# Kernel tuning notes

Hardware: AMD Instinct MI355X
Metric: run time of the kernel (lower is better)

Reference implementation:

```python
import jax, jax.numpy as jnp
import numpy as np

N_NODES = 50000
N_EDGES = 800000
IN_DIM, HID_DIM, N_CLASS = 128, 128, 2
DROPOUT_P = 0.5
NEG_SLOPE = 0.01  # F.leaky_relu default


def gcn_conv(x, src, dst, W, b, n_nodes):
    """PyG GCNConv: add self-loops, sym-normalize, aggregate, then bias."""
    loops = jnp.arange(n_nodes, dtype=src.dtype)
    s = jnp.concatenate([src, loops])
    d = jnp.concatenate([dst, loops])
    # degree on A + I (edge weights = 1), counted at destination
    deg = jax.ops.segment_sum(jnp.ones_like(d, dtype=x.dtype), d, num_segments=n_nodes)
    dis = jnp.where(deg > 0, jax.lax.rsqrt(deg), 0.0)  # deg^{-1/2}
    norm = dis[s] * dis[d]                               # [E+N]
    h = x @ W                                            # [N, out]
    msg = h[s] * norm[:, None]                           # gather + scale
    out = jax.ops.segment_sum(msg, d, num_segments=n_nodes)  # scatter-add
    return out + b


def dropout(x, p, key):
    keep = 1.0 - p
    mask = jax.random.bernoulli(key, keep, x.shape)
    return jnp.where(mask, x / keep, 0.0)


def setup_inputs() -> dict:
    key = jax.random.key(0)
    ks = jax.random.split(key, 8)
    x = jax.random.normal(ks[0], (N_NODES, IN_DIM), dtype=jnp.float32)
    edge_index = jax.random.randint(ks[1], (2, N_EDGES), 0, N_NODES, dtype=jnp.int64)
    def glorot(k, fin, fout):
        lim = np.sqrt(6.0 / (fin + fout)).astype(np.float32)
        return jax.random.uniform(k, (fin, fout), jnp.float32, -lim, lim)
    W1 = glorot(ks[2], IN_DIM, HID_DIM)
    W2 = glorot(ks[3], HID_DIM, HID_DIM)
    W3 = glorot(ks[4], HID_DIM, N_CLASS)
    b1 = jnp.zeros((HID_DIM,), jnp.float32)
    b2 = jnp.zeros((HID_DIM,), jnp.float32)
    b3 = jnp.zeros((N_CLASS,), jnp.float32)
    return {"x": x, "edge_index": edge_index, "W1": W1, "b1": b1,
            "W2": W2, "b2": b2, "W3": W3, "b3": b3}


def reference(x, edge_index, W1, b1, W2, b2, W3, b3):
    src, dst = edge_index[0], edge_index[1]
    n = x.shape[0]
    dkey = jax.random.key(42)
    k1, k2 = jax.random.split(dkey)
    h = gcn_conv(x, src, dst, W1, b1, n)
    h = jax.nn.leaky_relu(h, NEG_SLOPE)
    h = dropout(h, DROPOUT_P, k1)
    h = gcn_conv(h, src, dst, W2, b2, n)
    h = jax.nn.leaky_relu(h, NEG_SLOPE)
    h = dropout(h, DROPOUT_P, k2)
    h = gcn_conv(h, src, dst, W3, b3, n)
    return jax.nn.log_softmax(h, axis=1)
```

## Files before the change

### kernel.cpp

```cpp
#include <hip/hip_runtime.h>
#include <stdint.h>

#define N_NODES 50000
#define N_EDGES 800000
#define DIM     128
#define NB   196
#define CAP  8192
#define CHUNK 2048
#define NBLK 391
#define GCAP 4096
#define G3CAP 8192

typedef __attribute__((ext_vector_type(8))) unsigned short ushort8_t;
typedef __attribute__((ext_vector_type(8))) short bfrag;
typedef __attribute__((ext_vector_type(4))) float f32x4;

__host__ __device__ inline void threefry2x32(uint32_t k0, uint32_t k1,
                                             uint32_t x0, uint32_t x1,
                                             uint32_t& o0, uint32_t& o1) {
    uint32_t ks0 = k0, ks1 = k1, ks2 = k0 ^ k1 ^ 0x1BD11BDAu;
    uint32_t v0 = x0 + ks0, v1 = x1 + ks1;
#define TF_R(r) { v0 += v1; v1 = (v1 << (r)) | (v1 >> (32 - (r))); v1 ^= v0; }
    TF_R(13) TF_R(15) TF_R(26) TF_R(6)
    v0 += ks1; v1 += ks2 + 1u;
    TF_R(17) TF_R(29) TF_R(16) TF_R(24)
    v0 += ks2; v1 += ks0 + 2u;
    TF_R(13) TF_R(15) TF_R(26) TF_R(6)
    v0 += ks0; v1 += ks1 + 3u;
    TF_R(17) TF_R(29) TF_R(16) TF_R(24)
    v0 += ks1; v1 += ks2 + 4u;
    TF_R(13) TF_R(15) TF_R(26) TF_R(6)
    v0 += ks2; v1 += ks0 + 5u;
#undef TF_R
    o0 = v0; o1 = v1;
}

__device__ inline float drop_scale(uint32_t kk0, uint32_t kk1, uint32_t i) {
    uint32_t b0, b1;
    threefry2x32(kk0, kk1, 0u, i, b0, b1);
    uint32_t bits = b0 ^ b1;
    return (bits >> 31) ? 0.0f : 2.0f;
}

__device__ inline float bf2f(ushort u) {
    return __uint_as_float(((uint32_t)u) << 16);
}

__device__ inline ushort f2bf_rne(float f) {
    uint32_t bits = __float_as_uint(f);
    uint32_t lsb = (bits >> 16) & 1u;
    bits += 0x7fffu + lsb;
    return (ushort)(bits >> 16);
}

template<int F32A>
__device__ inline void gemm_body(const ushort* __restrict__ Xb,
                                 const float* __restrict__ Xf,
                                 const ushort* __restrict__ Wt,
                                 const float* __restrict__ dis,
                                 ushort* __restrict__ Hb, int gb, int tid) {
    int w = tid >> 6, lane = tid & 63;
    int m0 = gb * 128 + w * 32;
    int lrow = lane & 15, quad = lane >> 4;
    f32x4 acc[2][8] = {};
    for (int kt = 0; kt < DIM; kt += 32) {
        bfrag a[2], b[8];
        #pragma unroll
        for (int t = 0; t < 2; ++t) {
            int m = m0 + t * 16 + lrow;
            if (m >= N_NODES) m = 0;
            if (F32A) {
                const float* p = Xf + (size_t)m * DIM + kt + quad * 8;
                f32x4 v0 = *(const f32x4*)p;
                f32x4 v1 = *(const f32x4*)(p + 4);
                #pragma unroll
                for (int j = 0; j < 4; ++j) {
                    a[t][j]     = (short)f2bf_rne(v0[j]);
                    a[t][j + 4] = (short)f2bf_rne(v1[j]);
                }
            } else {
                a[t] = *(const bfrag*)(Xb + (size_t)m * DIM + kt + quad * 8);
            }
        }
        #pragma unroll
        for (int c = 0; c < 8; ++c) {
            int n = c * 16 + lrow;
            b[c] = *(const bfrag*)(Wt + (size_t)n * DIM + kt + quad * 8);
        }
        #pragma unroll
        for (int t = 0; t < 2; ++t)
            #pragma unroll
            for (int c = 0; c < 8; ++c)
                acc[t][c] = __builtin_amdgcn_mfma_f32_16x16x32_bf16(a[t], b[c], acc[t][c], 0, 0, 0);
    }
    #pragma unroll
    for (int t = 0; t < 2; ++t) {
        #pragma unroll
        for (int r = 0; r < 4; ++r) {
            int rowi = m0 + t * 16 + quad * 4 + r;
            if (rowi < N_NODES) {
                float dv = dis[rowi];
                #pragma unroll
                for (int c = 0; c < 8; ++c) {
                    int feat = c * 16 + lrow;
                    int fp = feat >> 5, off = feat & 31;
                    Hb[((size_t)fp * N_NODES + rowi) * 32 + off] = f2bf_rne(acc[t][c][r] * dv);
                }
            }
        }
    }
}

__global__ __launch_bounds__(256) void k_prep(const float* __restrict__ W1,
                                              const float* __restrict__ W2,
                                              ushort* __restrict__ W1t,
                                              ushort* __restrict__ W2t,
                                              const int* __restrict__ src,
                                              const int* __restrict__ dst,
                                              uint32_t* __restrict__ gcur,
                                              uint32_t* __restrict__ packed) {
    __shared__ uint32_t h[NB];
    int b = blockIdx.x;
    int t = threadIdx.x;
    if (b < NBLK) {
        uint32_t dc[CHUNK / 256], sc[CHUNK / 256];
        if (t < NB) h[t] = 0u;
        __syncthreads();
        int base = b * CHUNK;
        #pragma unroll
        for (int i = 0; i < CHUNK / 256; ++i) {
            int e = base + i * 256 + t;
            if (e < N_EDGES) {
                dc[i] = (uint32_t)dst[e];
                sc[i] = (uint32_t)src[e];
                atomicAdd(&h[dc[i] >> 8], 1u);
            } else {
                dc[i] = 0xffffffffu;
            }
        }
        __syncthreads();
        if (t < NB) {
            uint32_t c = h[t];
            h[t] = c ? atomicAdd(&gcur[t], c) : 0u;
        }
        __syncthreads();
        #pragma unroll
        for (int i = 0; i < CHUNK / 256; ++i) {
            if (dc[i] != 0xffffffffu) {
                uint32_t d = dc[i];
                uint32_t s = sc[i];
                uint32_t bk = d >> 8;
                uint32_t pos = atomicAdd(&h[bk], 1u);
                if (pos < CAP)
                    packed[(size_t)bk * CAP + pos] = ((d & 255u) << 16) | s;
            }
        }
    } else {
        int j = (b - NBLK) * 256 + t;
        const float* W = (j < DIM * DIM) ? W1 : W2;
        ushort* Wt = (j < DIM * DIM) ? W1t : W2t;
        int i = j & (DIM * DIM - 1);
        int k = i >> 7, n = i & 127;
        Wt[n * DIM + k] = f2bf_rne(W[k * DIM + n]);
    }
}

__global__ __launch_bounds__(256) void k_fill(const uint32_t* __restrict__ gcur,
                                              const uint32_t* __restrict__ packed,
                                              uint32_t* __restrict__ row,
                                              float* __restrict__ dis,
                                              ushort* __restrict__ col16) {
    __shared__ uint32_t sdeg[256];
    __shared__ uint32_t scan[256];
    __shared__ uint32_t cur[256];
    int b = blockIdx.x;
    int t = threadIdx.x;
    uint32_t n = gcur[b];
    scan[t] = (t < b) ? gcur[t] : 0u;
    __syncthreads();
    for (int off = 1; off < 256; off <<= 1) {
        uint32_t x = (t >= off) ? scan[t - off] : 0u;
        __syncthreads();
        scan[t] += x;
        __syncthreads();
    }
    uint32_t cbase = scan[255];
    __syncthreads();
    uint32_t pbase = (uint32_t)b * CAP;
    sdeg[t] = 0u;
    __syncthreads();
    for (uint32_t i = t; i < n; i += 256) {
        uint32_t u = packed[pbase + i];
        atomicAdd(&sdeg[u >> 16], 1u);
    }
    __syncthreads();
    uint32_t myd = sdeg[t];
    scan[t] = myd;
    __syncthreads();
    for (int off = 1; off < 256; off <<= 1) {
        uint32_t x = (t >= off) ? scan[t - off] : 0u;
        __syncthreads();
        scan[t] += x;
        __syncthreads();
    }
    uint32_t excl = scan[t] - myd;
    cur[t] = excl;
    int v = b * 256 + t;
    if (v <= N_NODES) row[v] = cbase + excl;
    if (v < N_NODES)  dis[v] = 1.0f / sqrtf((float)(myd + 1u));
    __syncthreads();
    for (uint32_t i = t; i < n; i += 256) {
        uint32_t u = packed[pbase + i];
        uint32_t pos = cbase + atomicAdd(&cur[u >> 16], 1u);
        col16[pos] = (ushort)(u & 0xffffu);
    }
}

template<int CLS>
__global__ __launch_bounds__(256) void k_gather_t(const uint32_t* __restrict__ row,
                                                  const ushort* __restrict__ col16,
                                                  const float* __restrict__ dis,
                                                  const ushort* __restrict__ Hb,
                                                  const float* __restrict__ bias,
                                                  ushort* __restrict__ OUTb,
                                                  const float* __restrict__ W3,
                                                  float* __restrict__ h3s,
                                                  uint32_t kk0, uint32_t kk1) {
    __shared__ ushort scol[GCAP];
    __shared__ uint32_t srow[65];
    int fp = blockIdx.x & 3;
    int c = blockIdx.x >> 2;
    int tid = threadIdx.x;
    int nbase = c * 64;
    int nend = nbase + 64; if (nend > N_NODES) nend = N_NODES;
    int nloc = nend - nbase;
    for (int i = tid; i <= nloc; i += 256) srow[i] = row[nbase + i];
    __syncthreads();
    uint32_t eLo = srow[0];
    uint32_t count = srow[nloc] - eLo;
    bool staged = count <= GCAP;
    if (staged) {
        for (uint32_t i = tid; i < count; i += 256) scol[i] = col16[eLo + i];
    }
    __syncthreads();

    int nl = tid >> 2;
    int q  = tid & 3;
    int v = nbase + nl;
    if (v >= N_NODES) return;
    const ushort* Hf = Hb + (size_t)fp * N_NODES * 32;
    ushort8_t hv = *((const ushort8_t*)(Hf + (size_t)v * 32 + q * 8));
    float acc[8];
    #pragma unroll
    for (int j = 0; j < 8; ++j) acc[j] = bf2f(hv[j]);

    uint32_t e0 = srow[nl] - eLo, e1 = srow[nl + 1] - eLo;
    uint32_t e = e0;
    if (staged) {
        for (; e + 4 <= e1; e += 4) {
            uint32_t s0 = scol[e], s1 = scol[e + 1], s2 = scol[e + 2], s3 = scol[e + 3];
            ushort8_t h0 = *((const ushort8_t*)(Hf + (size_t)s0 * 32 + q * 8));
            ushort8_t h1 = *((const ushort8_t*)(Hf + (size_t)s1 * 32 + q * 8));
            ushort8_t h2 = *((const ushort8_t*)(Hf + (size_t)s2 * 32 + q * 8));
            ushort8_t h3 = *((const ushort8_t*)(Hf + (size_t)s3 * 32 + q * 8));
            #pragma unroll
            for (int j = 0; j < 8; ++j)
                acc[j] += (bf2f(h0[j]) + bf2f(h1[j])) + (bf2f(h2[j]) + bf2f(h3[j]));
        }
        for (; e < e1; ++e) {
            uint32_t s0 = scol[e];
            ushort8_t h0 = *((const ushort8_t*)(Hf + (size_t)s0 * 32 + q * 8));
            #pragma unroll
            for (int j = 0; j < 8; ++j) acc[j] += bf2f(h0[j]);
        }
    } else {
        for (; e < e1; ++e) {
            uint32_t s0 = col16[eLo + e];
            ushort8_t h0 = *((const ushort8_t*)(Hf + (size_t)s0 * 32 + q * 8));
            #pragma unroll
            for (int j = 0; j < 8; ++j) acc[j] += bf2f(h0[j]);
        }
    }

    float dv = dis[v];
    int cbase = fp * 32 + q * 8;
    uint32_t ibase = (uint32_t)(v * DIM + cbase);
    if (CLS == 0) {
        ushort8_t o;
        #pragma unroll
        for (int j = 0; j < 8; ++j) {
            float z = acc[j] * dv + bias[cbase + j];
            z = (z >= 0.f) ? z : 0.01f * z;
            z *= drop_scale(kk0, kk1, ibase + j);
            o[j] = f2bf_rne(z);
        }
        *((ushort8_t*)(OUTb + (size_t)v * DIM + cbase)) = o;
    } else {
        float o0 = 0.f, o1 = 0.f;
        #pragma unroll
        for (int j = 0; j < 8; ++j) {
            float z = acc[j] * dv + bias[cbase + j];
            z = (z >= 0.f) ? z : 0.01f * z;
            z *= drop_scale(kk0, kk1, ibase + j);
            o0 += z * W3[(cbase + j) * 2 + 0];
            o1 += z * W3[(cbase + j) * 2 + 1];
        }
        o0 += __shfl_xor(o0, 1); o0 += __shfl_xor(o0, 2);
        o1 += __shfl_xor(o1, 1); o1 += __shfl_xor(o1, 2);
        if (q == 0) {
            atomicAdd(&h3s[v * 2 + 0], o0 * dv);
            atomicAdd(&h3s[v * 2 + 1], o1 * dv);
        }
    }
}

__global__ __launch_bounds__(256) void k_gemm_f32(const float* __restrict__ Xf,
                                                  const ushort* __restrict__ Wt,
                                                  const float* __restrict__ dis,
                                                  ushort* __restrict__ Hb) {
    gemm_body<1>(nullptr, Xf, Wt, dis, Hb, blockIdx.x, threadIdx.x);
}
__global__ __launch_bounds__(256) void k_gemm_bf16(const ushort* __restrict__ Xb,
                                                   const ushort* __restrict__ Wt,
                                                   const float* __restrict__ dis,
                                                   ushort* __restrict__ Hb) {
    gemm_body<0>(Xb, nullptr, Wt, dis, Hb, blockIdx.x, threadIdx.x);
}

__global__ __launch_bounds__(256) void k_gather3(const uint32_t* __restrict__ row,
                                                 const ushort* __restrict__ col16,
                                                 const float* __restrict__ dis,
                                                 const float* __restrict__ H3s,
                                                 const float* __restrict__ b3,
                                                 float* __restrict__ out) {
    __shared__ ushort scol[G3CAP];
    __shared__ uint32_t srow[257];
    int tid = threadIdx.x;
    int nbase = blockIdx.x * 256;
    int nend = nbase + 256; if (nend > N_NODES) nend = N_NODES;
    int nloc = nend - nbase;
    for (int i = tid; i <= nloc; i += 256) srow[i] = row[nbase + i];
    __syncthreads();
    uint32_t eLo = srow[0];
    uint32_t count = srow[nloc] - eLo;
    bool staged = count <= G3CAP;
    if (staged) {
        for (uint32_t i = tid; i < count; i += 256) scol[i] = col16[eLo + i];
    }
    __syncthreads();

    int v = nbase + tid;
    if (v >= N_NODES) return;
    const float2* H2 = (const float2*)H3s;
    float2 h = H2[v];
    float z0 = h.x, z1 = h.y;
    uint32_t e0 = srow[tid] - eLo, e1 = srow[tid + 1] - eLo;
    uint32_t e = e0;
    if (staged) {
        for (; e + 2 <= e1; e += 2) {
            float2 ha = H2[scol[e]];
            float2 hb = H2[scol[e + 1]];
            z0 += ha.x + hb.x; z1 += ha.y + hb.y;
        }
        if (e < e1) {
            float2 ha = H2[scol[e]];
            z0 += ha.x; z1 += ha.y;
        }
    } else {
        for (; e < e1; ++e) {
            float2 ha = H2[col16[eLo + e]];
            z0 += ha.x; z1 += ha.y;
        }
    }
    float dv = dis[v];
    z0 = z0 * dv + b3[0];
    z1 = z1 * dv + b3[1];
    float m = fmaxf(z0, z1);
    float lse = m + logf(expf(z0 - m) + expf(z1 - m));
    out[v * 2 + 0] = z0 - lse;
    out[v * 2 + 1] = z1 - lse;
}

extern "C" void kernel_launch(void* const* d_in, const int* in_sizes, int n_in,
                              void* d_out, int out_size, void* d_ws, size_t ws_size,
                              hipStream_t stream) {
    const float* x  = (const float*)d_in[0];
    const int*   ei = (const int*)d_in[1];
    const float* W1 = (const float*)d_in[2];
    const float* b1 = (const float*)d_in[3];
    const float* W2 = (const float*)d_in[4];
    const float* b2 = (const float*)d_in[5];
    const float* W3 = (const float*)d_in[6];
    const float* b3 = (const float*)d_in[7];
    float* out = (float*)d_out;

    const int* src = ei;
    const int* dst = ei + N_EDGES;

    uint32_t* wsu = (uint32_t*)d_ws;
    float*    wsf = (float*)d_ws;
    uint32_t* gcur   = wsu;
    uint32_t* row    = wsu + 256;
    float*    dis    = wsf + 50304;
    uint32_t* packed = wsu + 100352;
    ushort*   col16  = (ushort*)(wsu + 1705984);
    ushort*   Hb     = (ushort*)(wsu + 2106112);
    ushort*   Bb     = (ushort*)(wsu + 8506112);
    ushort*   W1t    = (ushort*)(wsu + 11706112);
    ushort*   W2t    = (ushort*)(wsu + 11714304);
    float*    h3s    = wsf + 11722496;

    uint32_t k1a, k1b, k2a, k2b;
    threefry2x32(0u, 42u, 0u, 0u, k1a, k1b);
    threefry2x32(0u, 42u, 0u, 1u, k2a, k2b);

    hipMemsetAsync(gcur, 0, 256 * sizeof(uint32_t), stream);
    hipMemsetAsync(h3s, 0, N_NODES * 2 * sizeof(float), stream);

    k_prep<<<NBLK + 128, 256, 0, stream>>>(W1, W2, W1t, W2t,
                                           src, dst, gcur, packed);

    k_fill<<<NB, 256, 0, stream>>>(gcur, packed, row, dis, col16);

    int mgrid = (N_NODES + 127) / 128;
    int ggrid = ((N_NODES + 63) / 64) * 4;

    k_gemm_f32<<<mgrid, 256, 0, stream>>>(x, W1t, dis, Hb);
    k_gather_t<0><<<ggrid, 256, 0, stream>>>(row, col16, dis, Hb, b1, Bb,
                                             nullptr, nullptr, k1a, k1b);

    k_gemm_bf16<<<mgrid, 256, 0, stream>>>(Bb, W2t, dis, Hb);
    k_gather_t<1><<<ggrid, 256, 0, stream>>>(row, col16, dis, Hb, b2, nullptr,
                                             W3, h3s, k2a, k2b);

    k_gather3<<<(N_NODES + 255) / 256, 256, 0, stream>>>(row, col16, dis, h3s, b3, out);
}
```

Baseline: 223.6 us.

## Fuse layer-1 GEMM into fill kernel, use row-major H and 16-node gather blocks

The layer-1 GEMM no longer needs the degree normalisation, so it runs as extra blocks inside the CSR fill kernel and that launch is gone. The source-side dis scaling moves into the first gather, which reads dis per neighbour. The h3s memset is folded into the prep kernel as extra zeroing blocks. H changes from a feature-partitioned layout to plain row-major, and each gather block now covers 16 nodes with 16 lanes per node instead of 64 nodes split across 4 feature blocks. In exchange, the first gather does an extra scattered dis load and multiply per edge, and each neighbour row is fetched as one contiguous 256-byte read rather than 64-byte slices.

After: 215.3 us. -3.7%, faster.

```diff
diff --git a/kernel.cpp b/kernel.cpp
--- a/kernel.cpp
+++ b/kernel.cpp
@@ -8,8 +8,11 @@
 #define CAP  8192
 #define CHUNK 2048
 #define NBLK 391
-#define GCAP 4096
+#define GNODES 16
+#define GGRID 3125
+#define GCAP2 2048
 #define G3CAP 8192
+#define ZBLK 98
 
 typedef __attribute__((ext_vector_type(8))) unsigned short ushort8_t;
 typedef __attribute__((ext_vector_type(8))) short bfrag;
@@ -53,7 +56,7 @@
     return (ushort)(bits >> 16);
 }
 
-template<int F32A>
+template<int F32A, int SCALE>
 __device__ inline void gemm_body(const ushort* __restrict__ Xb,
                                  const float* __restrict__ Xf,
                                  const ushort* __restrict__ Wt,
@@ -99,12 +102,12 @@
         for (int r = 0; r < 4; ++r) {
             int rowi = m0 + t * 16 + quad * 4 + r;
             if (rowi < N_NODES) {
-                float dv = dis[rowi];
+                float dv = SCALE ? dis[rowi] : 1.0f;
                 #pragma unroll
                 for (int c = 0; c < 8; ++c) {
                     int feat = c * 16 + lrow;
-                    int fp = feat >> 5, off = feat & 31;
-                    Hb[((size_t)fp * N_NODES + rowi) * 32 + off] = f2bf_rne(acc[t][c][r] * dv);
+                    float z = SCALE ? acc[t][c][r] * dv : acc[t][c][r];
+                    Hb[(size_t)rowi * DIM + feat] = f2bf_rne(z);
                 }
             }
         }
@@ -118,7 +121,8 @@
                                               const int* __restrict__ src,
                                               const int* __restrict__ dst,
                                               uint32_t* __restrict__ gcur,
-                                              uint32_t* __restrict__ packed) {
+                                              uint32_t* __restrict__ packed,
+                                              float* __restrict__ h3s) {
     __shared__ uint32_t h[NB];
     int b = blockIdx.x;
     int t = threadIdx.x;
@@ -155,13 +159,19 @@
                     packed[(size_t)bk * CAP + pos] = ((d & 255u) << 16) | s;
             }
         }
-    } else {
+    } else if (b < NBLK + 128) {
         int j = (b - NBLK) * 256 + t;
         const float* W = (j < DIM * DIM) ? W1 : W2;
         ushort* Wt = (j < DIM * DIM) ? W1t : W2t;
         int i = j & (DIM * DIM - 1);
         int k = i >> 7, n = i & 127;
         Wt[n * DIM + k] = f2bf_rne(W[k * DIM + n]);
+    } else {
+        int idx = (b - NBLK - 128) * 256 + t;
+        if (idx < (N_NODES * 2) / 4) {
+            f32x4 z = {0.f, 0.f, 0.f, 0.f};
+            ((f32x4*)h3s)[idx] = z;
+        }
     }
 }
 
@@ -169,19 +179,26 @@
                                               const uint32_t* __restrict__ packed,
                                               uint32_t* __restrict__ row,
                                               float* __restrict__ dis,
-                                              ushort* __restrict__ col16) {
+                                              ushort* __restrict__ col16,
+                                              const float* __restrict__ x,
+                                              const ushort* __restrict__ W1t,
+                                              ushort* __restrict__ Hb) {
     __shared__ uint32_t sdeg[256];
     __shared__ uint32_t scan[256];
     __shared__ uint32_t cur[256];
     int b = blockIdx.x;
     int t = threadIdx.x;
+    if (b >= NB) {
+        gemm_body<1, 0>(nullptr, x, W1t, nullptr, Hb, b - NB, t);
+        return;
+    }
     uint32_t n = gcur[b];
     scan[t] = (t < b) ? gcur[t] : 0u;
     __syncthreads();
     for (int off = 1; off < 256; off <<= 1) {
-        uint32_t x = (t >= off) ? scan[t - off] : 0u;
-        __syncthreads();
-        scan[t] += x;
+        uint32_t xx = (t >= off) ? scan[t - off] : 0u;
+        __syncthreads();
+        scan[t] += xx;
         __syncthreads();
     }
     uint32_t cbase = scan[255];
@@ -198,9 +215,9 @@
     scan[t] = myd;
     __syncthreads();
     for (int off = 1; off < 256; off <<= 1) {
-        uint32_t x = (t >= off) ? scan[t - off] : 0u;
-        __syncthreads();
-        scan[t] += x;
+        uint32_t xx = (t >= off) ? scan[t - off] : 0u;
+        __syncthreads();
+        scan[t] += xx;
         __syncthreads();
     }
     uint32_t excl = scan[t] - myd;
@@ -216,7 +233,7 @@
     }
 }
 
-template<int CLS>
+template<int CLS, int SRCDIS>
 __global__ __launch_bounds__(256) void k_gather_t(const uint32_t* __restrict__ row,
                                                   const ushort* __restrict__ col16,
                                                   const float* __restrict__ dis,
@@ -226,64 +243,71 @@
                                                   const float* __restrict__ W3,
                                                   float* __restrict__ h3s,
                                                   uint32_t kk0, uint32_t kk1) {
-    __shared__ ushort scol[GCAP];
-    __shared__ uint32_t srow[65];
-    int fp = blockIdx.x & 3;
-    int c = blockIdx.x >> 2;
+    __shared__ ushort scol[GCAP2];
+    __shared__ uint32_t srow[GNODES + 1];
     int tid = threadIdx.x;
-    int nbase = c * 64;
-    int nend = nbase + 64; if (nend > N_NODES) nend = N_NODES;
-    int nloc = nend - nbase;
-    for (int i = tid; i <= nloc; i += 256) srow[i] = row[nbase + i];
+    int nbase = blockIdx.x * GNODES;
+    if (tid <= GNODES) srow[tid] = row[nbase + tid];
     __syncthreads();
     uint32_t eLo = srow[0];
-    uint32_t count = srow[nloc] - eLo;
-    bool staged = count <= GCAP;
+    uint32_t count = srow[GNODES] - eLo;
+    bool staged = count <= GCAP2;
     if (staged) {
         for (uint32_t i = tid; i < count; i += 256) scol[i] = col16[eLo + i];
     }
     __syncthreads();
 
-    int nl = tid >> 2;
-    int q  = tid & 3;
+    int nl = tid >> 4;
+    int q  = tid & 15;
     int v = nbase + nl;
-    if (v >= N_NODES) return;
-    const ushort* Hf = Hb + (size_t)fp * N_NODES * 32;
-    ushort8_t hv = *((const ushort8_t*)(Hf + (size_t)v * 32 + q * 8));
+    float dv = dis[v];
+    ushort8_t hv = *((const ushort8_t*)(Hb + (size_t)v * DIM + q * 8));
     float acc[8];
     #pragma unroll
-    for (int j = 0; j < 8; ++j) acc[j] = bf2f(hv[j]);
+    for (int j = 0; j < 8; ++j)
+        acc[j] = SRCDIS ? dv * bf2f(hv[j]) : bf2f(hv[j]);
 
     uint32_t e0 = srow[nl] - eLo, e1 = srow[nl + 1] - eLo;
     uint32_t e = e0;
     if (staged) {
         for (; e + 4 <= e1; e += 4) {
             uint32_t s0 = scol[e], s1 = scol[e + 1], s2 = scol[e + 2], s3 = scol[e + 3];
-            ushort8_t h0 = *((const ushort8_t*)(Hf + (size_t)s0 * 32 + q * 8));
-            ushort8_t h1 = *((const ushort8_t*)(Hf + (size_t)s1 * 32 + q * 8));
-            ushort8_t h2 = *((const ushort8_t*)(Hf + (size_t)s2 * 32 + q * 8));
-            ushort8_t h3 = *((const ushort8_t*)(Hf + (size_t)s3 * 32 + q * 8));
+            ushort8_t h0 = *((const ushort8_t*)(Hb + (size_t)s0 * DIM + q * 8));
+            ushort8_t h1 = *((const ushort8_t*)(Hb + (size_t)s1 * DIM + q * 8));
+            ushort8_t h2 = *((const ushort8_t*)(Hb + (size_t)s2 * DIM + q * 8));
+            ushort8_t h3 = *((const ushort8_t*)(Hb + (size_t)s3 * DIM + q * 8));
+            if (SRCDIS) {
+                float d0 = dis[s0], d1 = dis[s1], d2 = dis[s2], d3 = dis[s3];
+                #pragma unroll
+                for (int j = 0; j < 8; ++j)
+                    acc[j] += d0 * bf2f(h0[j]) + d1 * bf2f(h1[j])
+                            + d2 * bf2f(h2[j]) + d3 * bf2f(h3[j]);
+            } else {
+                #pragma unroll
+                for (int j = 0; j < 8; ++j)
+                    acc[j] += (bf2f(h0[j]) + bf2f(h1[j])) + (bf2f(h2[j]) + bf2f(h3[j]));
+            }
+        }
+        for (; e < e1; ++e) {
+            uint32_t s0 = scol[e];
+            ushort8_t h0 = *((const ushort8_t*)(Hb + (size_t)s0 * DIM + q * 8));
+            float d0 = SRCDIS ? dis[s0] : 1.0f;
             #pragma unroll
             for (int j = 0; j < 8; ++j)
-                acc[j] += (bf2f(h0[j]) + bf2f(h1[j])) + (bf2f(h2[j]) + bf2f(h3[j]));
-        }
-        for (; e < e1; ++e) {
-            uint32_t s0 = scol[e];
-            ushort8_t h0 = *((const ushort8_t*)(Hf + (size_t)s0 * 32 + q * 8));
-            #pragma unroll
-            for (int j = 0; j < 8; ++j) acc[j] += bf2f(h0[j]);
+                acc[j] += SRCDIS ? d0 * bf2f(h0[j]) : bf2f(h0[j]);
         }
     } else {
         for (; e < e1; ++e) {
             uint32_t s0 = col16[eLo + e];
-            ushort8_t h0 = *((const ushort8_t*)(Hf + (size_t)s0 * 32 + q * 8));
+            ushort8_t h0 = *((const ushort8_t*)(Hb + (size_t)s0 * DIM + q * 8));
+            float d0 = SRCDIS ? dis[s0] : 1.0f;
             #pragma unroll
-            for (int j = 0; j < 8; ++j) acc[j] += bf2f(h0[j]);
-        }
-    }
-
-    float dv = dis[v];
-    int cbase = fp * 32 + q * 8;
+            for (int j = 0; j < 8; ++j)
+                acc[j] += SRCDIS ? d0 * bf2f(h0[j]) : bf2f(h0[j]);
+        }
+    }
+
+    int cbase = q * 8;
     uint32_t ibase = (uint32_t)(v * DIM + cbase);
     if (CLS == 0) {
         ushort8_t o;
@@ -306,7 +330,9 @@
             o1 += z * W3[(cbase + j) * 2 + 1];
         }
         o0 += __shfl_xor(o0, 1); o0 += __shfl_xor(o0, 2);
+        o0 += __shfl_xor(o0, 4); o0 += __shfl_xor(o0, 8);
         o1 += __shfl_xor(o1, 1); o1 += __shfl_xor(o1, 2);
+        o1 += __shfl_xor(o1, 4); o1 += __shfl_xor(o1, 8);
         if (q == 0) {
             atomicAdd(&h3s[v * 2 + 0], o0 * dv);
             atomicAdd(&h3s[v * 2 + 1], o1 * dv);
@@ -314,17 +340,11 @@
     }
 }
 
-__global__ __launch_bounds__(256) void k_gemm_f32(const float* __restrict__ Xf,
-                                                  const ushort* __restrict__ Wt,
-                                                  const float* __restrict__ dis,
-                                                  ushort* __restrict__ Hb) {
-    gemm_body<1>(nullptr, Xf, Wt, dis, Hb, blockIdx.x, threadIdx.x);
-}
 __global__ __launch_bounds__(256) void k_gemm_bf16(const ushort* __restrict__ Xb,
                                                    const ushort* __restrict__ Wt,
                                                    const float* __restrict__ dis,
                                                    ushort* __restrict__ Hb) {
-    gemm_body<0>(Xb, nullptr, Wt, dis, Hb, blockIdx.x, threadIdx.x);
+    gemm_body<0, 1>(Xb, nullptr, Wt, dis, Hb, blockIdx.x, threadIdx.x);
 }
 
 __global__ __launch_bounds__(256) void k_gather3(const uint32_t* __restrict__ row,
@@ -415,23 +435,19 @@
     threefry2x32(0u, 42u, 0u, 1u, k2a, k2b);
 
     hipMemsetAsync(gcur, 0, 256 * sizeof(uint32_t), stream);
-    hipMemsetAsync(h3s, 0, N_NODES * 2 * sizeof(float), stream);
-
-    k_prep<<<NBLK + 128, 256, 0, stream>>>(W1, W2, W1t, W2t,
-                                           src, dst, gcur, packed);
-
-    k_fill<<<NB, 256, 0, stream>>>(gcur, packed, row, dis, col16);
-
-    int mgrid = (N_NODES + 127) / 128;
-    int ggrid = ((N_NODES + 63) / 64) * 4;
-
-    k_gemm_f32<<<mgrid, 256, 0, stream>>>(x, W1t, dis, Hb);
-    k_gather_t<0><<<ggrid, 256, 0, stream>>>(row, col16, dis, Hb, b1, Bb,
-                                             nullptr, nullptr, k1a, k1b);
-
-    k_gemm_bf16<<<mgrid, 256, 0, stream>>>(Bb, W2t, dis, Hb);
-    k_gather_t<1><<<ggrid, 256, 0, stream>>>(row, col16, dis, Hb, b2, nullptr,
-                                             W3, h3s, k2a, k2b);
+
+    k_prep<<<NBLK + 128 + ZBLK, 256, 0, stream>>>(W1, W2, W1t, W2t,
+                                                  src, dst, gcur, packed, h3s);
+
+    k_fill<<<NB + 391, 256, 0, stream>>>(gcur, packed, row, dis, col16,
+                                         x, W1t, Hb);
+
+    k_gather_t<0, 1><<<GGRID, 256, 0, stream>>>(row, col16, dis, Hb, b1, Bb,
+                                                nullptr, nullptr, k1a, k1b);
+
+    k_gemm_bf16<<<(N_NODES + 127) / 128, 256, 0, stream>>>(Bb, W2t, dis, Hb);
+    k_gather_t<1, 0><<<GGRID, 256, 0, stream>>>(row, col16, dis, Hb, b2, nullptr,
+                                                W3, h3s, k2a, k2b);
 
     k_gather3<<<(N_NODES + 255) / 256, 256, 0, stream>>>(row, col16, dis, h3s, b3, out);
 }
```
